# Kernel tuning notes

Measured on AMD Instinct MI355X. Metric: run time of the kernel, lower is better.

## Reference

```python
import jax, jax.numpy as jnp
import numpy as np

# Mamba2 config (matches mamba_ssm.Mamba2 defaults used by the wrapper)
D_MODEL = 1024
D_STATE = 128
D_CONV = 4
EXPAND = 2
HEADDIM = 64
CHUNK = 256
D_INNER = EXPAND * D_MODEL            # 2048
NHEADS = D_INNER // HEADDIM           # 32
CONV_DIM = D_INNER + 2 * D_STATE      # 2304 (x, B, C share the causal conv)
D_IN_PROJ = 2 * D_INNER + 2 * D_STATE + NHEADS  # z, xBC, dt
EPS = 1e-5


def rmsnorm(x, w, eps=EPS):
    return x * jax.lax.rsqrt(jnp.mean(x * x, axis=-1, keepdims=True) + eps) * w


def setup_inputs() -> dict:
    key = jax.random.key(0)
    ks = jax.random.split(key, 8)
    B, L = 2, 2048
    def w(k, shape, sc=0.02):
        return jax.random.normal(k, shape, jnp.float32) * sc
    return {
        "x": jax.random.normal(ks[0], (B, L, D_MODEL), jnp.float32),
        "norm_w": jnp.ones((D_MODEL,), jnp.float32),
        "in_proj_w": w(ks[1], (D_IN_PROJ, D_MODEL)),
        "conv_w": w(ks[2], (CONV_DIM, 1, D_CONV), 0.2),   # depthwise kernel
        "conv_b": jnp.zeros((CONV_DIM,), jnp.float32),
        "dt_bias": w(ks[3], (NHEADS,), 1.0),
        "A_log": jnp.log(1.0 + 15.0 * jax.random.uniform(ks[4], (NHEADS,), jnp.float32)),
        "D": jnp.ones((NHEADS,), jnp.float32),
        "gnorm_w": jnp.ones((D_INNER,), jnp.float32),
        "out_proj_w": w(ks[5], (D_MODEL, D_INNER)),
    }


def _ssd(xd, a, Bm, Cm):
    """Chunked SSD scan (ssd_minimal_discrete).
    xd: (b,l,h,p) = x*dt ; a: (b,l,h) = dt*A ; Bm,Cm: (b,l,n) (ngroups=1)."""
    b, l, h, p = xd.shape
    n = Bm.shape[-1]
    nc = l // CHUNK
    xd = xd.reshape(b, nc, CHUNK, h, p)
    a = a.reshape(b, nc, CHUNK, h).transpose(0, 3, 1, 2)   # (b,h,nc,c)
    Bm = Bm.reshape(b, nc, CHUNK, n)
    Cm = Cm.reshape(b, nc, CHUNK, n)
    a_cs = jnp.cumsum(a, axis=-1)                           # (b,h,nc,c)
    # 1) intra-chunk: causal decay matrix L[t,s] = exp(sum_{s<i<=t} a_i)
    diff = a_cs[..., :, None] - a_cs[..., None, :]          # (b,h,nc,c,c)
    mask = jnp.tril(jnp.ones((CHUNK, CHUNK), bool))
    Lm = jnp.exp(jnp.where(mask, diff, 0.0)) * mask
    Y_diag = jnp.einsum("bcln,bcsn,bhcls,bcshp->bclhp", Cm, Bm, Lm, xd)
    # 2) per-chunk end states
    decay_states = jnp.exp(a_cs[..., -1:] - a_cs)           # (b,h,nc,c)
    states = jnp.einsum("bcln,bhcl,bclhp->bchpn", Bm, decay_states, xd)
    # 3) inter-chunk recurrence (vectorized segsum over the 8+1 chunk totals)
    tot = jnp.pad(a_cs[..., -1], ((0, 0), (0, 0), (1, 0)))  # (b,h,nc+1)
    tot_cs = jnp.cumsum(tot, axis=-1)
    dchunk = tot_cs[..., :, None] - tot_cs[..., None, :]    # (b,h,nc+1,nc+1)
    cmask = jnp.tril(jnp.ones((nc + 1, nc + 1), bool))
    dchunk = jnp.exp(jnp.where(cmask, dchunk, 0.0)) * cmask
    states = jnp.concatenate([jnp.zeros_like(states[:, :1]), states], axis=1)
    new_states = jnp.einsum("bhzc,bchpn->bzhpn", dchunk, states)
    init_states = new_states[:, :-1]                        # state entering each chunk
    # 4) state -> output contribution
    Y_off = jnp.einsum("bcln,bchpn,bhcl->bclhp", Cm, init_states, jnp.exp(a_cs))
    return (Y_diag + Y_off).reshape(b, l, h, p)


def reference(x, norm_w, in_proj_w, conv_w, conv_b, dt_bias, A_log, D, gnorm_w, out_proj_w):
    res = x
    u = rmsnorm(x, norm_w)
    zxbcdt = u @ in_proj_w.T                                # (b,l,d_in_proj)
    z, xBC, dt = jnp.split(zxbcdt, [D_INNER, D_INNER + CONV_DIM], axis=-1)
    # causal depthwise conv1d over (x,B,C), then SiLU
    xBC_t = jnp.pad(xBC.transpose(0, 2, 1), ((0, 0), (0, 0), (D_CONV - 1, 0)))
    conv = jax.lax.conv_general_dilated(
        xBC_t, conv_w, (1,), "VALID",
        dimension_numbers=("NCH", "OIH", "NCH"), feature_group_count=CONV_DIM)
    xBC = jax.nn.silu(conv.transpose(0, 2, 1) + conv_b)
    xs, Bm, Cm = jnp.split(xBC, [D_INNER, D_INNER + D_STATE], axis=-1)
    dt = jax.nn.softplus(dt + dt_bias)                      # (b,l,h)
    A = -jnp.exp(A_log)                                     # (h,)
    xh = xs.reshape(xs.shape[0], xs.shape[1], NHEADS, HEADDIM)
    y = _ssd(xh * dt[..., None], dt * A, Bm, Cm)
    y = y + D[None, None, :, None] * xh                     # skip term
    y = y.reshape(xs.shape)
    y = rmsnorm(y * jax.nn.silu(z), gnorm_w)                # gated RMSNorm
    return res + y @ out_proj_w.T
```

## Files before the change

### kernel.cpp

```cpp
#include <hip/hip_runtime.h>
#include <hip/hip_bf16.h>

typedef __hip_bfloat16 bf16_t;
typedef __attribute__((ext_vector_type(8))) short bfrag8;
typedef __attribute__((ext_vector_type(4))) float floatx4;

#define DM     1024
#define DI     2048
#define NHD    32
#define HD     64
#define DSTATE 128
#define CONVD  2304
#define NPROJ  4384
#define NPAD   4480
#define MR     4096
#define LL     2048
#define EPSF   1e-5f
#define PSTR   40

__device__ __forceinline__ void gl_lds16(const void* g, void* l) {
  __builtin_amdgcn_global_load_lds((const __attribute__((address_space(1))) void*)g,
                                   (__attribute__((address_space(3))) void*)l, 16, 0, 0);
}
__device__ __forceinline__ unsigned pack_bf16_rn(float a, float b) {
  unsigned ua = (__float_as_uint(a) + 0x8000u) >> 16;
  unsigned ub = (__float_as_uint(b) + 0x8000u) >> 16;
  return ua | (ub << 16);
}
__device__ __forceinline__ unsigned short bf16u(float a) {
  return (unsigned short)((__float_as_uint(a) + 0x8000u) >> 16);
}
__device__ __forceinline__ float blo(unsigned u){ return __uint_as_float(u << 16); }
__device__ __forceinline__ float bhi(unsigned u){ return __uint_as_float(u & 0xffff0000u); }
__device__ __forceinline__ void unp8(uint4 u, float* v) {
  v[0]=blo(u.x); v[1]=bhi(u.x); v[2]=blo(u.y); v[3]=bhi(u.y);
  v[4]=blo(u.z); v[5]=bhi(u.z); v[6]=blo(u.w); v[7]=bhi(u.w);
}

__global__ void rms1_kernel(const float* __restrict__ x, const float* __restrict__ w,
                            bf16_t* __restrict__ ub) {
  int row = blockIdx.x, t = threadIdx.x;
  float4 v = ((const float4*)(x + (long)row * DM))[t];
  float ss = v.x*v.x + v.y*v.y + v.z*v.z + v.w*v.w;
#pragma unroll
  for (int off = 32; off > 0; off >>= 1) ss += __shfl_down(ss, off, 64);
  __shared__ float red[4];
  if ((t & 63) == 0) red[t >> 6] = ss;
  __syncthreads();
  float tot = red[0] + red[1] + red[2] + red[3];
  float rs = rsqrtf(tot * (1.f / DM) + EPSF);
  float4 wv = ((const float4*)w)[t];
  bf16_t* o = ub + (long)row * DM + t * 4;
  o[0] = __float2bfloat16(v.x * rs * wv.x);
  o[1] = __float2bfloat16(v.y * rs * wv.y);
  o[2] = __float2bfloat16(v.z * rs * wv.z);
  o[3] = __float2bfloat16(v.w * rs * wv.w);
}

#define W1CNT (NPAD * DM / 4)
#define W2CNT (DM * DI / 4)
__global__ void cvtw_kernel(const float* __restrict__ w1, const float* __restrict__ w2,
                            bf16_t* __restrict__ o1, bf16_t* __restrict__ o2) {
  int i4 = blockIdx.x * 256 + threadIdx.x;
  if (i4 < W1CNT) {
    int idx = i4 * 4;
    int row = idx >> 10;
    float4 v = make_float4(0.f, 0.f, 0.f, 0.f);
    if (row < NPROJ) v = *(const float4*)(w1 + idx);
    bf16_t* d = o1 + idx;
    d[0] = __float2bfloat16(v.x); d[1] = __float2bfloat16(v.y);
    d[2] = __float2bfloat16(v.z); d[3] = __float2bfloat16(v.w);
  } else {
    int idx = (i4 - W1CNT) * 4;
    float4 v = *(const float4*)(w2 + idx);
    bf16_t* d = o2 + idx;
    d[0] = __float2bfloat16(v.x); d[1] = __float2bfloat16(v.y);
    d[2] = __float2bfloat16(v.z); d[3] = __float2bfloat16(v.w);
  }
}

template<int TN, bool DO_RES, bool OUT_BF16>
__global__ __launch_bounds__(256) void gemm64_kernel(const bf16_t* __restrict__ A,
    const bf16_t* __restrict__ Bw, const float* __restrict__ resid,
    void* __restrict__ Cout, int N, int K) {
  __shared__ bf16_t As[128 * 64];
  __shared__ bf16_t Bs[TN * 64];
  const int tid = threadIdx.x;
  const int lane = tid & 63;
  const int wv = tid >> 6;
  const int l15 = lane & 15;
  const int l4 = lane >> 4;
  constexpr int MF = (TN == 128) ? 4 : 2;
  const int wm = (TN == 128) ? ((wv >> 1) << 6) : (wv << 5);
  const int wn = (TN == 128) ? ((wv & 1) << 6) : 0;
  const int tm = blockIdx.x << 7;
  const int tn = blockIdx.y * TN;

  floatx4 acc[MF][4];
#pragma unroll
  for (int i = 0; i < MF; i++)
#pragma unroll
    for (int j = 0; j < 4; j++) acc[i][j] = (floatx4){0.f, 0.f, 0.f, 0.f};

  const int r = tid >> 3;
  const int c8 = tid & 7;
  const int scol = ((c8 ^ (r & 7)) << 3);
  const bf16_t* Ag = A + (long)(tm + r) * K + scol;
  const bf16_t* Bg = Bw + (long)(tn + r) * K + scol;
  const int swz = l15 & 7;

  for (int k0 = 0; k0 < K; k0 += 64) {
#pragma unroll
    for (int q = 0; q < 4; q++)
      gl_lds16(Ag + (long)(q * 32) * K + k0, &As[q * 2048 + tid * 8]);
#pragma unroll
    for (int q = 0; q < TN / 32; q++)
      gl_lds16(Bg + (long)(q * 32) * K + k0, &Bs[q * 2048 + tid * 8]);
    __syncthreads();
#pragma unroll
    for (int kk = 0; kk < 2; kk++) {
      bfrag8 af[MF], bfr[4];
      const int ch = ((kk << 2) | l4) ^ swz;
#pragma unroll
      for (int j = 0; j < 4; j++)
        bfr[j] = *(const bfrag8*)&Bs[(wn + j * 16 + l15) * 64 + ch * 8];
#pragma unroll
      for (int i = 0; i < MF; i++)
        af[i] = *(const bfrag8*)&As[(wm + i * 16 + l15) * 64 + ch * 8];
#pragma unroll
      for (int i = 0; i < MF; i++)
#pragma unroll
        for (int j = 0; j < 4; j++)
          acc[i][j] = __builtin_amdgcn_mfma_f32_16x16x32_bf16(af[i], bfr[j], acc[i][j], 0, 0, 0);
    }
    __syncthreads();
  }
#pragma unroll
  for (int i = 0; i < MF; i++)
#pragma unroll
    for (int j = 0; j < 4; j++)
#pragma unroll
      for (int r2 = 0; r2 < 4; r2++) {
        int row = tm + wm + i * 16 + l4 * 4 + r2;
        int col = tn + wn + j * 16 + l15;
        float v = acc[i][j][r2];
        if (OUT_BF16) {
          ((bf16_t*)Cout)[(long)row * N + col] = __float2bfloat16(v);
        } else {
          if (DO_RES) v += resid[(long)row * N + col];
          ((float*)Cout)[(long)row * N + col] = v;
        }
      }
}

__global__ __launch_bounds__(256) void gemm_s_kernel(const bf16_t* __restrict__ Cmh,
                const bf16_t* __restrict__ Bmh, float* __restrict__ SL) {
  __shared__ bf16_t As[128 * 32];
  __shared__ bf16_t Bs[128 * 32];
  const int tid = threadIdx.x;
  const int lane = tid & 63;
  const int wv = tid >> 6;
  const int wm = (wv >> 1) << 6;
  const int wn = (wv & 1) << 6;
  const int bc = blockIdx.z;
  const int tm = blockIdx.x << 7;
  const int tn = blockIdx.y << 7;
  const int l15 = lane & 15;
  const int l4 = lane >> 4;
  floatx4 acc[4][4];
#pragma unroll
  for (int i = 0; i < 4; i++)
#pragma unroll
    for (int j = 0; j < 4; j++) acc[i][j] = (floatx4){0.f, 0.f, 0.f, 0.f};
  const int arow = tid >> 2;
  const int acol = (tid & 3) << 3;
  const bf16_t* Ag = Cmh + (long)bc * 256 * DSTATE + (long)(tm + arow) * DSTATE + acol;
  const bf16_t* Bg = Bmh + (long)bc * 256 * DSTATE + (long)(tn + arow) * DSTATE + acol;
  const long k64 = (long)64 * DSTATE;
  for (int k0 = 0; k0 < DSTATE; k0 += 32) {
    gl_lds16(Ag + k0, &As[tid * 8]);
    gl_lds16(Ag + k64 + k0, &As[2048 + tid * 8]);
    gl_lds16(Bg + k0, &Bs[tid * 8]);
    gl_lds16(Bg + k64 + k0, &Bs[2048 + tid * 8]);
    __syncthreads();
    bfrag8 af[4], bfr[4];
#pragma unroll
    for (int i = 0; i < 4; i++)
      af[i] = *(const bfrag8*)&As[(wm + i * 16 + l15) * 32 + l4 * 8];
#pragma unroll
    for (int j = 0; j < 4; j++)
      bfr[j] = *(const bfrag8*)&Bs[(wn + j * 16 + l15) * 32 + l4 * 8];
#pragma unroll
    for (int i = 0; i < 4; i++)
#pragma unroll
      for (int j = 0; j < 4; j++)
        acc[i][j] = __builtin_amdgcn_mfma_f32_16x16x32_bf16(af[i], bfr[j], acc[i][j], 0, 0, 0);
    __syncthreads();
  }
  float* Cb = SL + (long)bc * 65536;
#pragma unroll
  for (int i = 0; i < 4; i++)
#pragma unroll
    for (int j = 0; j < 4; j++)
#pragma unroll
      for (int r = 0; r < 4; r++)
        Cb[(long)(tm + wm + i * 16 + l4 * 4 + r) * 256 + tn + wn + j * 16 + l15] = acc[i][j][r];
}

__global__ __launch_bounds__(256) void conv4_kernel(const bf16_t* __restrict__ zxh,
    const float* __restrict__ cw, const float* __restrict__ cb,
    bf16_t* __restrict__ xhb, bf16_t* __restrict__ Bmh, bf16_t* __restrict__ Cmh) {
  int g = blockIdx.x * 256 + threadIdx.x;
  int cg = g % 288;
  int blt = g / 288;
  int c0 = cg * 8;
  long bl0 = (long)blt * 4;
  int l0 = (int)(bl0 & (LL - 1));
  const bf16_t* base = zxh + bl0 * NPAD + DI + c0;
  float rv[7][8];
#pragma unroll
  for (int j = 0; j < 7; j++) {
    int dj = j - 3;
    if (l0 + dj >= 0) {
      uint4 u = *(const uint4*)(base + (long)dj * NPAD);
      unp8(u, rv[j]);
    } else {
#pragma unroll
      for (int q = 0; q < 8; q++) rv[j][q] = 0.f;
    }
  }
  float4 wq[8];
#pragma unroll
  for (int q = 0; q < 8; q++) wq[q] = ((const float4*)cw)[c0 + q];
  float bias[8];
  *(float4*)&bias[0] = *(const float4*)(cb + c0);
  *(float4*)&bias[4] = *(const float4*)(cb + c0 + 4);
#pragma unroll
  for (int i = 0; i < 4; i++) {
    unsigned o[4];
#pragma unroll
    for (int q2 = 0; q2 < 4; q2++) {
      float rr[2];
#pragma unroll
      for (int e = 0; e < 2; e++) {
        int q = q2 * 2 + e;
        float a = bias[q] + wq[q].x * rv[i][q] + wq[q].y * rv[i + 1][q]
                + wq[q].z * rv[i + 2][q] + wq[q].w * rv[i + 3][q];
        rr[e] = a / (1.f + __expf(-a));
      }
      o[q2] = pack_bf16_rn(rr[0], rr[1]);
    }
    uint4 ov = make_uint4(o[0], o[1], o[2], o[3]);
    long bl = bl0 + i;
    if (c0 < DI)               *(uint4*)(xhb + bl * DI + c0) = ov;
    else if (c0 < DI + DSTATE) *(uint4*)(Bmh + bl * DSTATE + (c0 - DI)) = ov;
    else                       *(uint4*)(Cmh + bl * DSTATE + (c0 - DI - DSTATE)) = ov;
  }
}

__global__ void acs_kernel(const bf16_t* __restrict__ zxh, const float* __restrict__ A_log,
                           const float* __restrict__ dtb,
                           float* __restrict__ acs, float* __restrict__ ctot,
                           float* __restrict__ dtout) {
  int blk = blockIdx.x;
  int h = blk & 31, bc = blk >> 5;
  int t = threadIdx.x, lane = t & 63, w = t >> 6;
  float Ah = -__expf(A_log[h]);
  int gl = bc * 256 + t;
  float vv = __bfloat162float(zxh[(long)gl * NPAD + (NPROJ - 32) + h]) + dtb[h];
  float sp = fmaxf(vv, 0.f) + log1pf(__expf(-fabsf(vv)));
  dtout[gl * 32 + h] = sp;
  float a = sp * Ah;
#pragma unroll
  for (int off = 1; off < 64; off <<= 1) {
    float v = __shfl_up(a, off, 64);
    if (lane >= off) a += v;
  }
  __shared__ float wsum[4];
  if (lane == 63) wsum[w] = a;
  __syncthreads();
  float base = 0.f;
  for (int i = 0; i < 4; i++) base += (i < w) ? wsum[i] : 0.f;
  a += base;
  acs[blk * 256 + t] = a;
  if (t == 255) ctot[blk] = a;
}

__global__ __launch_bounds__(256) void xdt_kernel(const bf16_t* __restrict__ xhb,
    const bf16_t* __restrict__ Bmh, const float* __restrict__ dt,
    const float* __restrict__ acs, bf16_t* __restrict__ xdT,
    bf16_t* __restrict__ xdTe, bf16_t* __restrict__ BmT) {
  __shared__ unsigned short Tb[9216];
  int blk = blockIdx.x;
  int t = threadIdx.x;
  if (blk < 512) {
    unsigned short* T1 = Tb;
    unsigned short* T2 = Tb + 4608;
    int h = blk & 31, bc = blk >> 5;
    float atot = acs[blk * 256 + 255];
    int l_loc = t >> 2, pg = t & 3;
    for (int lt = 0; lt < 4; lt++) {
      int gl = bc * 256 + lt * 64 + l_loc;
      float w1 = dt[gl * 32 + h];
      float w2 = w1 * __expf(atot - acs[blk * 256 + lt * 64 + l_loc]);
      const uint4* src = (const uint4*)(xhb + (long)gl * DI + h * HD + pg * 16);
      uint4 u0 = src[0], u1 = src[1];
      float v[16];
      unp8(u0, v); unp8(u1, v + 8);
      __syncthreads();
#pragma unroll
      for (int q = 0; q < 16; q++) {
        T1[(pg * 16 + q) * 72 + l_loc] = bf16u(v[q] * w1);
        T2[(pg * 16 + q) * 72 + l_loc] = bf16u(v[q] * w2);
      }
      __syncthreads();
      long orow = ((long)blk * 64 + l_loc) * 256 + lt * 64 + pg * 16;
      *(uint4*)(xdT + orow)      = *(uint4*)&T1[l_loc * 72 + pg * 16];
      *(uint4*)(xdT + orow + 8)  = *(uint4*)&T1[l_loc * 72 + pg * 16 + 8];
      *(uint4*)(xdTe + orow)     = *(uint4*)&T2[l_loc * 72 + pg * 16];
      *(uint4*)(xdTe + orow + 8) = *(uint4*)&T2[l_loc * 72 + pg * 16 + 8];
    }
  } else {
    unsigned short* T = Tb;
    int bc = blk - 512;
    int l_loc = t >> 2, ng = t & 3;
    for (int lt = 0; lt < 4; lt++) {
      int gl = bc * 256 + lt * 64 + l_loc;
      const uint4* src = (const uint4*)(Bmh + (long)gl * DSTATE + ng * 32);
      uint4 u[4];
#pragma unroll
      for (int q = 0; q < 4; q++) u[q] = src[q];
      __syncthreads();
      const unsigned short* us = (const unsigned short*)u;
#pragma unroll
      for (int e = 0; e < 32; e++)
        T[(ng * 32 + e) * 72 + l_loc] = us[e];
      __syncthreads();
      int n = t >> 1, lg2 = t & 1;
      long orow = ((long)bc * 128 + n) * 256 + lt * 64 + lg2 * 32;
#pragma unroll
      for (int q = 0; q < 4; q++)
        *(uint4*)(BmT + orow + q * 8) = *(uint4*)&T[n * 72 + lg2 * 32 + q * 8];
    }
  }
}

__global__ __launch_bounds__(256) void states3_kernel(const bf16_t* __restrict__ xdTe,
    const bf16_t* __restrict__ BmT, bf16_t* __restrict__ states) {
  int blk = blockIdx.x;
  int bc = blk >> 5;
  int t = threadIdx.x, lane = t & 63, wv = t >> 6;
  int l15 = lane & 15, l4 = lane >> 4;
  floatx4 acc[2][4];
#pragma unroll
  for (int i = 0; i < 2; i++)
#pragma unroll
    for (int j = 0; j < 4; j++) acc[i][j] = (floatx4){0.f, 0.f, 0.f, 0.f};
  const bf16_t* arow = BmT + (long)bc * 128 * 256;
  const bf16_t* brow = xdTe + (long)blk * 64 * 256;
#pragma unroll
  for (int kt = 0; kt < 8; kt++) {
    bfrag8 af[2], bfr[4];
#pragma unroll
    for (int i = 0; i < 2; i++)
      af[i] = *(const bfrag8*)(arow + (long)(wv * 32 + i * 16 + l15) * 256 + kt * 32 + l4 * 8);
#pragma unroll
    for (int j = 0; j < 4; j++)
      bfr[j] = *(const bfrag8*)(brow + (long)(j * 16 + l15) * 256 + kt * 32 + l4 * 8);
#pragma unroll
    for (int i = 0; i < 2; i++)
#pragma unroll
      for (int j = 0; j < 4; j++)
        acc[i][j] = __builtin_amdgcn_mfma_f32_16x16x32_bf16(af[i], bfr[j], acc[i][j], 0, 0, 0);
  }
#pragma unroll
  for (int i = 0; i < 2; i++)
#pragma unroll
    for (int j = 0; j < 4; j++) {
      int n_base = wv * 32 + i * 16 + l4 * 4;
      int p = j * 16 + l15;
      unsigned lo = pack_bf16_rn(acc[i][j][0], acc[i][j][1]);
      unsigned hi = pack_bf16_rn(acc[i][j][2], acc[i][j][3]);
      *(uint2*)(states + (long)blk * 8192 + p * 128 + n_base) = make_uint2(lo, hi);
    }
}

__global__ void scan_kernel(const bf16_t* __restrict__ states, const float* __restrict__ ctot,
                            bf16_t* __restrict__ initsb) {
  int id = blockIdx.x * 256 + threadIdx.x;
  int pn = id & 8191;
  int bh = id >> 13;
  int b = bh >> 5, h = bh & 31;
  float S = 0.f;
#pragma unroll
  for (int c = 0; c < 8; c++) {
    int blk = (b * 8 + c) * 32 + h;
    initsb[(long)blk * 8192 + pn] = __float2bfloat16(S);
    S = __expf(ctot[blk]) * S + __bfloat162float(states[(long)blk * 8192 + pn]);
  }
}

__global__ __launch_bounds__(256, 4) void yk2_kernel(const float* __restrict__ SL,
     const bf16_t* __restrict__ Cmh, const bf16_t* __restrict__ xhb,
     const bf16_t* __restrict__ zxh, const float* __restrict__ acs,
     const bf16_t* __restrict__ initsb, const bf16_t* __restrict__ xdT,
     const float* __restrict__ Dp, bf16_t* __restrict__ yg, float* __restrict__ ssqp) {
  int bi = blockIdx.x;
  int mh = bi & 1, h = (bi >> 1) & 31, bc = bi >> 6;
  int ablk = bc * 32 + h;
  int t = threadIdx.x;
  int lane = t & 63, wv = t >> 6;
  int l15 = lane & 15, l4 = lane >> 4;
  __shared__ float acsS[256];
  __shared__ __align__(16) char ubuf[128 * 66 * 4];
  bf16_t* Ps = (bf16_t*)ubuf;
  float* Yt = (float*)ubuf;

  acsS[t] = acs[ablk * 256 + t];
  __syncthreads();
  const int l_loc = t >> 1, half = t & 1;
  const int l = mh * 128 + l_loc;
  const float al = acsS[l];
  const float eAl = __expf(al);
  const int rowbase = bc * 256;
  const float* SLb = SL + (long)bc * 65536 + (long)l * 256;
  const bf16_t* xrow = xdT + (long)ablk * 64 * 256;

  floatx4 acc[2][4];
#pragma unroll
  for (int i = 0; i < 2; i++)
#pragma unroll
    for (int j = 0; j < 4; j++) acc[i][j] = (floatx4){0.f, 0.f, 0.f, 0.f};

  const int nkd = (mh + 1) * 4;
  for (int kt = 0; kt < nkd + 4; kt++) {
    __syncthreads();
    if (kt < nkd) {
      int s0 = kt * 32 + half * 16;
      unsigned pk[8];
      const float4* Sg = (const float4*)(SLb + s0);
#pragma unroll
      for (int q = 0; q < 4; q++) {
        float4 v = Sg[q];
        int sb = s0 + q * 4;
        float p0 = (sb + 0 <= l) ? v.x * __expf(al - acsS[sb + 0]) : 0.f;
        float p1 = (sb + 1 <= l) ? v.y * __expf(al - acsS[sb + 1]) : 0.f;
        float p2 = (sb + 2 <= l) ? v.z * __expf(al - acsS[sb + 2]) : 0.f;
        float p3 = (sb + 3 <= l) ? v.w * __expf(al - acsS[sb + 3]) : 0.f;
        pk[q * 2 + 0] = pack_bf16_rn(p0, p1);
        pk[q * 2 + 1] = pack_bf16_rn(p2, p3);
      }
      uint4* pw = (uint4*)&Ps[l_loc * PSTR + half * 16];
      pw[0] = make_uint4(pk[0], pk[1], pk[2], pk[3]);
      pw[1] = make_uint4(pk[4], pk[5], pk[6], pk[7]);
    } else {
      int n0 = (kt - nkd) * 32;
      unsigned pk[8];
      const uint4* Cg = (const uint4*)(Cmh + (long)(rowbase + l) * DSTATE + n0 + half * 16);
      uint4 u0 = Cg[0], u1 = Cg[1];
      float cv[16];
      unp8(u0, cv); unp8(u1, cv + 8);
#pragma unroll
      for (int q = 0; q < 8; q++)
        pk[q] = pack_bf16_rn(cv[q * 2] * eAl, cv[q * 2 + 1] * eAl);
      uint4* pw = (uint4*)&Ps[l_loc * PSTR + half * 16];
      pw[0] = make_uint4(pk[0], pk[1], pk[2], pk[3]);
      pw[1] = make_uint4(pk[4], pk[5], pk[6], pk[7]);
    }
    __syncthreads();
    bfrag8 bfr[4];
    if (kt < nkd) {
#pragma unroll
      for (int j = 0; j < 4; j++)
        bfr[j] = *(const bfrag8*)(xrow + (long)(j * 16 + l15) * 256 + kt * 32 + l4 * 8);
    } else {
      int n0 = (kt - nkd) * 32;
#pragma unroll
      for (int j = 0; j < 4; j++)
        bfr[j] = *(const bfrag8*)(initsb + (long)ablk * 8192 + (j * 16 + l15) * 128 + n0 + l4 * 8);
    }
#pragma unroll
    for (int i = 0; i < 2; i++) {
      bfrag8 af = *(const bfrag8*)&Ps[(wv * 32 + i * 16 + l15) * PSTR + l4 * 8];
#pragma unroll
      for (int j = 0; j < 4; j++)
        acc[i][j] = __builtin_amdgcn_mfma_f32_16x16x32_bf16(af, bfr[j], acc[i][j], 0, 0, 0);
    }
  }
  __syncthreads();
#pragma unroll
  for (int i = 0; i < 2; i++)
#pragma unroll
    for (int j = 0; j < 4; j++)
#pragma unroll
      for (int r = 0; r < 4; r++)
        Yt[(wv * 32 + i * 16 + l4 * 4 + r) * 66 + j * 16 + l15] = acc[i][j][r];
  __syncthreads();
  {
    int row_l = t >> 1;
    int ch = (t & 1) * 32;
    long rowg = rowbase + mh * 128 + row_l;
    float Dh = Dp[h];
    float ss = 0.f;
#pragma unroll
    for (int it = 0; it < 4; it++) {
      int c = ch + it * 8;
      float4 y0 = *(const float4*)&Yt[row_l * 66 + c];
      float4 y1 = *(const float4*)&Yt[row_l * 66 + c + 4];
      uint4 ux = *(const uint4*)(xhb + rowg * DI + h * HD + c);
      uint4 uz = *(const uint4*)(zxh + rowg * NPAD + h * HD + c);
      float xv[8], zv[8];
      unp8(ux, xv); unp8(uz, zv);
      float yv[8] = {y0.x, y0.y, y0.z, y0.w, y1.x, y1.y, y1.z, y1.w};
      unsigned o[4];
#pragma unroll
      for (int q = 0; q < 4; q++) {
        float v0 = (yv[q * 2 + 0] + Dh * xv[q * 2 + 0]) *
                   (zv[q * 2 + 0] / (1.f + __expf(-zv[q * 2 + 0])));
        float v1 = (yv[q * 2 + 1] + Dh * xv[q * 2 + 1]) *
                   (zv[q * 2 + 1] / (1.f + __expf(-zv[q * 2 + 1])));
        ss += v0 * v0 + v1 * v1;
        o[q] = pack_bf16_rn(v0, v1);
      }
      *(uint4*)(yg + rowg * DI + h * HD + c) = make_uint4(o[0], o[1], o[2], o[3]);
    }
    ss += __shfl_xor(ss, 1, 64);
    if ((t & 1) == 0) ssqp[rowg * 32 + h] = ss;
  }
}

__global__ void gnorm2_kernel(const bf16_t* __restrict__ yg, const float* __restrict__ ssqp,
                              const float* __restrict__ gw, bf16_t* __restrict__ yn) {
  int row = blockIdx.x, t = threadIdx.x;
  __shared__ float rsS;
  if (t < 64) {
    float v = (t < 32) ? ssqp[row * 32 + t] : 0.f;
#pragma unroll
    for (int off = 16; off > 0; off >>= 1) v += __shfl_down(v, off, 64);
    if (t == 0) rsS = rsqrtf(v * (1.f / DI) + EPSF);
  }
  __syncthreads();
  float rs = rsS;
  uint4 u = *(const uint4*)(yg + (long)row * DI + t * 8);
  float4 g0 = ((const float4*)gw)[t * 2];
  float4 g1 = ((const float4*)gw)[t * 2 + 1];
  unsigned o0 = pack_bf16_rn(blo(u.x) * rs * g0.x, bhi(u.x) * rs * g0.y);
  unsigned o1 = pack_bf16_rn(blo(u.y) * rs * g0.z, bhi(u.y) * rs * g0.w);
  unsigned o2 = pack_bf16_rn(blo(u.z) * rs * g1.x, bhi(u.z) * rs * g1.y);
  unsigned o3 = pack_bf16_rn(blo(u.w) * rs * g1.z, bhi(u.w) * rs * g1.w);
  *(uint4*)(yn + (long)row * DI + t * 8) = make_uint4(o0, o1, o2, o3);
}

extern "C" void kernel_launch(void* const* d_in, const int* in_sizes, int n_in,
                              void* d_out, int out_size, void* d_ws, size_t ws_size,
                              hipStream_t stream) {
  const float* x    = (const float*)d_in[0];
  const float* nw   = (const float*)d_in[1];
  const float* w1   = (const float*)d_in[2];
  const float* cw   = (const float*)d_in[3];
  const float* cb   = (const float*)d_in[4];
  const float* dtb  = (const float*)d_in[5];
  const float* alog = (const float*)d_in[6];
  const float* Dp   = (const float*)d_in[7];
  const float* gw   = (const float*)d_in[8];
  const float* w2   = (const float*)d_in[9];
  float* out = (float*)d_out;

  char* ws = (char*)d_ws;
  size_t off = 0;
  auto alloc = [&](size_t bytes) -> void* {
    void* p = ws + off;
    off += (bytes + 255) & ~(size_t)255;
    return p;
  };
  bf16_t* ub     = (bf16_t*)alloc((size_t)MR * DM * 2);
  bf16_t* w1b    = (bf16_t*)alloc((size_t)NPAD * DM * 2);
  bf16_t* w2b    = (bf16_t*)alloc((size_t)DM * DI * 2);
  bf16_t* zxh    = (bf16_t*)alloc((size_t)MR * NPAD * 2);
  bf16_t* xhb    = (bf16_t*)alloc((size_t)MR * DI * 2);
  bf16_t* Bmh    = (bf16_t*)alloc((size_t)MR * DSTATE * 2);
  bf16_t* Cmh    = (bf16_t*)alloc((size_t)MR * DSTATE * 2);
  float* SL      = (float*)alloc((size_t)16 * 256 * 256 * 4);
  float* dt      = (float*)alloc((size_t)MR * NHD * 4);
  float* acs     = (float*)alloc((size_t)512 * 256 * 4);
  float* ctot    = (float*)alloc((size_t)512 * 4);
  bf16_t* states = (bf16_t*)alloc((size_t)512 * 8192 * 2);
  bf16_t* initsb = (bf16_t*)alloc((size_t)512 * 8192 * 2);
  bf16_t* xdT    = (bf16_t*)alloc((size_t)512 * 64 * 256 * 2);
  bf16_t* xdTe   = (bf16_t*)alloc((size_t)512 * 64 * 256 * 2);
  bf16_t* BmT    = (bf16_t*)alloc((size_t)16 * 128 * 256 * 2);
  bf16_t* yg     = (bf16_t*)alloc((size_t)MR * DI * 2);
  float* ssqp    = (float*)alloc((size_t)MR * NHD * 4);
  bf16_t* yn     = (bf16_t*)alloc((size_t)MR * DI * 2);
  if (off > ws_size) return;

  rms1_kernel<<<MR, 256, 0, stream>>>(x, nw, ub);
  cvtw_kernel<<<(W1CNT + W2CNT) / 256, 256, 0, stream>>>(w1, w2, w1b, w2b);
  gemm64_kernel<128, false, true><<<dim3(MR / 128, NPAD / 128), 256, 0, stream>>>(
      ub, w1b, nullptr, zxh, NPAD, DM);
  conv4_kernel<<<(1024 * 288) / 256, 256, 0, stream>>>(zxh, cw, cb, xhb, Bmh, Cmh);
  acs_kernel<<<512, 256, 0, stream>>>(zxh, alog, dtb, acs, ctot, dt);
  xdt_kernel<<<528, 256, 0, stream>>>(xhb, Bmh, dt, acs, xdT, xdTe, BmT);
  gemm_s_kernel<<<dim3(2, 2, 16), 256, 0, stream>>>(Cmh, Bmh, SL);
  states3_kernel<<<512, 256, 0, stream>>>(xdTe, BmT, states);
  scan_kernel<<<(2 * 32 * 8192) / 256, 256, 0, stream>>>(states, ctot, initsb);
  yk2_kernel<<<1024, 256, 0, stream>>>(SL, Cmh, xhb, zxh, acs, initsb, xdT, Dp, yg, ssqp);
  gnorm2_kernel<<<MR, 256, 0, stream>>>(yg, ssqp, gw, yn);
  gemm64_kernel<64, true, false><<<dim3(MR / 128, DM / 64), 256, 0, stream>>>(
      yn, w2b, x, out, DM, DI);
}
```

Measured before the change: 296.8 us.

## Stage xdT and init states in swizzled LDS, prefetch SL, use exp2

The Y kernel now preloads the per-head xdT block and the initial-state block into LDS with async global-to-LDS loads, using an XOR swizzle to avoid bank conflicts, instead of reading B fragments straight from global memory on every k-step. It also prefetches the next SL row segment into registers while the current one is processed, and moves the barrier to the end of each iteration. Cumulative decays are pre-scaled by log2(e) so exp2f replaces __expf in the acs, xdt, scan and Y kernels. LDS use grows to about 58KB per block and the launch-bounds occupancy hint is dropped, which may reduce occupancy.

Result: faster. 290.6 us (-2.1%).

```diff
diff --git a/kernel.cpp b/kernel.cpp
--- a/kernel.cpp
+++ b/kernel.cpp
@@ -17,6 +17,7 @@
 #define LL     2048
 #define EPSF   1e-5f
 #define PSTR   40
+#define LOG2E  1.44269504088896f
 
 __device__ __forceinline__ void gl_lds16(const void* g, void* l) {
   __builtin_amdgcn_global_load_lds((const __attribute__((address_space(1))) void*)g,
@@ -265,7 +266,7 @@
   int blk = blockIdx.x;
   int h = blk & 31, bc = blk >> 5;
   int t = threadIdx.x, lane = t & 63, w = t >> 6;
-  float Ah = -__expf(A_log[h]);
+  float Ah = -__expf(A_log[h]) * LOG2E;
   int gl = bc * 256 + t;
   float vv = __bfloat162float(zxh[(long)gl * NPAD + (NPROJ - 32) + h]) + dtb[h];
   float sp = fmaxf(vv, 0.f) + log1pf(__expf(-fabsf(vv)));
@@ -302,7 +303,7 @@
     for (int lt = 0; lt < 4; lt++) {
       int gl = bc * 256 + lt * 64 + l_loc;
       float w1 = dt[gl * 32 + h];
-      float w2 = w1 * __expf(atot - acs[blk * 256 + lt * 64 + l_loc]);
+      float w2 = w1 * exp2f(atot - acs[blk * 256 + lt * 64 + l_loc]);
       const uint4* src = (const uint4*)(xhb + (long)gl * DI + h * HD + pg * 16);
       uint4 u0 = src[0], u1 = src[1];
       float v[16];
@@ -396,11 +397,11 @@
   for (int c = 0; c < 8; c++) {
     int blk = (b * 8 + c) * 32 + h;
     initsb[(long)blk * 8192 + pn] = __float2bfloat16(S);
-    S = __expf(ctot[blk]) * S + __bfloat162float(states[(long)blk * 8192 + pn]);
-  }
-}
-
-__global__ __launch_bounds__(256, 4) void yk2_kernel(const float* __restrict__ SL,
+    S = exp2f(ctot[blk]) * S + __bfloat162float(states[(long)blk * 8192 + pn]);
+  }
+}
+
+__global__ __launch_bounds__(256) void yk3_kernel(const float* __restrict__ SL,
      const bf16_t* __restrict__ Cmh, const bf16_t* __restrict__ xhb,
      const bf16_t* __restrict__ zxh, const float* __restrict__ acs,
      const bf16_t* __restrict__ initsb, const bf16_t* __restrict__ xdT,
@@ -412,19 +413,39 @@
   int lane = t & 63, wv = t >> 6;
   int l15 = lane & 15, l4 = lane >> 4;
   __shared__ float acsS[256];
-  __shared__ __align__(16) char ubuf[128 * 66 * 4];
-  bf16_t* Ps = (bf16_t*)ubuf;
-  float* Yt = (float*)ubuf;
-
+  __shared__ bf16_t Ps[128 * PSTR];
+  __shared__ __align__(16) char bbuf[49152];
+  bf16_t* xds = (bf16_t*)bbuf;
+  bf16_t* ins = (bf16_t*)(bbuf + 32768);
+  float* Yt = (float*)bbuf;
+
+  {
+    const bf16_t* xrow_g = xdT + (long)ablk * 64 * 256;
+#pragma unroll
+    for (int it = 0; it < 8; it++) {
+      int sl = it * 256 + t;
+      int p = sl >> 5, s = sl & 31;
+      int c = (s & 24) | ((s & 7) ^ (p & 7));
+      gl_lds16(xrow_g + p * 256 + c * 8, &xds[sl * 8]);
+    }
+    const bf16_t* irow_g = initsb + (long)ablk * 8192;
+#pragma unroll
+    for (int it = 0; it < 4; it++) {
+      int sl = it * 256 + t;
+      int p = sl >> 4, s = sl & 15;
+      int c = (s & 8) | ((s & 7) ^ (p & 7));
+      gl_lds16(irow_g + p * 128 + c * 8, &ins[sl * 8]);
+    }
+  }
   acsS[t] = acs[ablk * 256 + t];
   __syncthreads();
+
   const int l_loc = t >> 1, half = t & 1;
   const int l = mh * 128 + l_loc;
   const float al = acsS[l];
-  const float eAl = __expf(al);
+  const float eAl = exp2f(al);
   const int rowbase = bc * 256;
   const float* SLb = SL + (long)bc * 65536 + (long)l * 256;
-  const bf16_t* xrow = xdT + (long)ablk * 64 * 256;
 
   floatx4 acc[2][4];
 #pragma unroll
@@ -433,29 +454,27 @@
     for (int j = 0; j < 4; j++) acc[i][j] = (floatx4){0.f, 0.f, 0.f, 0.f};
 
   const int nkd = (mh + 1) * 4;
+  float4 slv[4];
+#pragma unroll
+  for (int q = 0; q < 4; q++) slv[q] = ((const float4*)(SLb + half * 16))[q];
+
   for (int kt = 0; kt < nkd + 4; kt++) {
-    __syncthreads();
+    unsigned pk[8];
     if (kt < nkd) {
       int s0 = kt * 32 + half * 16;
-      unsigned pk[8];
-      const float4* Sg = (const float4*)(SLb + s0);
 #pragma unroll
       for (int q = 0; q < 4; q++) {
-        float4 v = Sg[q];
+        float4 v = slv[q];
         int sb = s0 + q * 4;
-        float p0 = (sb + 0 <= l) ? v.x * __expf(al - acsS[sb + 0]) : 0.f;
-        float p1 = (sb + 1 <= l) ? v.y * __expf(al - acsS[sb + 1]) : 0.f;
-        float p2 = (sb + 2 <= l) ? v.z * __expf(al - acsS[sb + 2]) : 0.f;
-        float p3 = (sb + 3 <= l) ? v.w * __expf(al - acsS[sb + 3]) : 0.f;
+        float p0 = (sb + 0 <= l) ? v.x * exp2f(al - acsS[sb + 0]) : 0.f;
+        float p1 = (sb + 1 <= l) ? v.y * exp2f(al - acsS[sb + 1]) : 0.f;
+        float p2 = (sb + 2 <= l) ? v.z * exp2f(al - acsS[sb + 2]) : 0.f;
+        float p3 = (sb + 3 <= l) ? v.w * exp2f(al - acsS[sb + 3]) : 0.f;
         pk[q * 2 + 0] = pack_bf16_rn(p0, p1);
         pk[q * 2 + 1] = pack_bf16_rn(p2, p3);
       }
-      uint4* pw = (uint4*)&Ps[l_loc * PSTR + half * 16];
-      pw[0] = make_uint4(pk[0], pk[1], pk[2], pk[3]);
-      pw[1] = make_uint4(pk[4], pk[5], pk[6], pk[7]);
     } else {
       int n0 = (kt - nkd) * 32;
-      unsigned pk[8];
       const uint4* Cg = (const uint4*)(Cmh + (long)(rowbase + l) * DSTATE + n0 + half * 16);
       uint4 u0 = Cg[0], u1 = Cg[1];
       float cv[16];
@@ -463,21 +482,35 @@
 #pragma unroll
       for (int q = 0; q < 8; q++)
         pk[q] = pack_bf16_rn(cv[q * 2] * eAl, cv[q * 2 + 1] * eAl);
+    }
+    {
       uint4* pw = (uint4*)&Ps[l_loc * PSTR + half * 16];
       pw[0] = make_uint4(pk[0], pk[1], pk[2], pk[3]);
       pw[1] = make_uint4(pk[4], pk[5], pk[6], pk[7]);
     }
+    if (kt + 1 < nkd) {
+#pragma unroll
+      for (int q = 0; q < 4; q++)
+        slv[q] = ((const float4*)(SLb + (kt + 1) * 32 + half * 16))[q];
+    }
     __syncthreads();
     bfrag8 bfr[4];
     if (kt < nkd) {
-#pragma unroll
-      for (int j = 0; j < 4; j++)
-        bfr[j] = *(const bfrag8*)(xrow + (long)(j * 16 + l15) * 256 + kt * 32 + l4 * 8);
+      int ch = kt * 4 + l4;
+#pragma unroll
+      for (int j = 0; j < 4; j++) {
+        int p = j * 16 + l15;
+        int sw = (ch & 24) | ((ch & 7) ^ (p & 7));
+        bfr[j] = *(const bfrag8*)&xds[(p * 32 + sw) * 8];
+      }
     } else {
-      int n0 = (kt - nkd) * 32;
-#pragma unroll
-      for (int j = 0; j < 4; j++)
-        bfr[j] = *(const bfrag8*)(initsb + (long)ablk * 8192 + (j * 16 + l15) * 128 + n0 + l4 * 8);
+      int ch = (kt - nkd) * 4 + l4;
+#pragma unroll
+      for (int j = 0; j < 4; j++) {
+        int p = j * 16 + l15;
+        int sw = (ch & 8) | ((ch & 7) ^ (p & 7));
+        bfr[j] = *(const bfrag8*)&ins[(p * 16 + sw) * 8];
+      }
     }
 #pragma unroll
     for (int i = 0; i < 2; i++) {
@@ -486,8 +519,8 @@
       for (int j = 0; j < 4; j++)
         acc[i][j] = __builtin_amdgcn_mfma_f32_16x16x32_bf16(af, bfr[j], acc[i][j], 0, 0, 0);
     }
-  }
-  __syncthreads();
+    __syncthreads();
+  }
 #pragma unroll
   for (int i = 0; i < 2; i++)
 #pragma unroll
@@ -604,7 +637,7 @@
   gemm_s_kernel<<<dim3(2, 2, 16), 256, 0, stream>>>(Cmh, Bmh, SL);
   states3_kernel<<<512, 256, 0, stream>>>(xdTe, BmT, states);
   scan_kernel<<<(2 * 32 * 8192) / 256, 256, 0, stream>>>(states, ctot, initsb);
-  yk2_kernel<<<1024, 256, 0, stream>>>(SL, Cmh, xhb, zxh, acs, initsb, xdT, Dp, yg, ssqp);
+  yk3_kernel<<<1024, 256, 0, stream>>>(SL, Cmh, xhb, zxh, acs, initsb, xdT, Dp, yg, ssqp);
   gnorm2_kernel<<<MR, 256, 0, stream>>>(yg, ssqp, gw, yn);
   gemm64_kernel<64, true, false><<<dim3(MR / 128, DM / 64), 256, 0, stream>>>(
       yn, w2b, x, out, DM, DI);
```
